# Performance work log

Hardware: AMD Instinct MI355X
Metric: run time of the kernel (lower is better)

The kernel has to match this reference:

```python
import jax, jax.numpy as jnp
import numpy as np
from jax import lax

B, T, D = 4, 4096, 1024  # d_inner == D (expansion=1.0)


def setup_inputs() -> dict:
    key = jax.random.key(0)
    ks = jax.random.split(key, 6)
    s = 1.0 / np.sqrt(D)  # xavier-ish scale
    return {
        "x": jax.random.normal(ks[0], (B, T, D), dtype=jnp.float32),
        "W_in": jax.random.normal(ks[1], (D, D), dtype=jnp.float32) * s,
        "W_alpha": jax.random.normal(ks[2], (D, D), dtype=jnp.float32) * s,
        "b_alpha": jnp.full((D,), 2.0, dtype=jnp.float32),
        "W_beta": jax.random.normal(ks[3], (D, D), dtype=jnp.float32) * s,
        "b_beta": jnp.zeros((D,), dtype=jnp.float32),
        "W_v": jax.random.normal(ks[4], (D, D), dtype=jnp.float32) * s,
        "b_v": jnp.zeros((D,), dtype=jnp.float32),
        "W_out": jax.random.normal(ks[5], (D, D), dtype=jnp.float32) * s,
    }


def reference(x, W_in, W_alpha, b_alpha, W_beta, b_beta, W_v, b_v, W_out):
    # x: [B, T, D]; torch nn.Linear convention y = x @ W.T
    xp = jax.nn.silu(jnp.einsum("btd,ed->bte", x, W_in))  # [B, T, Di]
    alpha = jax.nn.sigmoid(jnp.einsum("bte,fe->btf", xp, W_alpha) + b_alpha)
    beta = jax.nn.sigmoid(jnp.einsum("bte,fe->btf", xp, W_beta) + b_beta)
    v = jnp.tanh(jnp.einsum("bte,fe->btf", xp, W_v) + b_v)
    bv = beta * v  # precompute write term

    def step(h, ab):
        a_t, bv_t = ab  # each [B, Di]
        h = a_t * h + bv_t
        return h, h * jax.nn.silu(h)

    h0 = jnp.zeros((x.shape[0], W_alpha.shape[0]), dtype=x.dtype)
    h_last, outs = lax.scan(step, h0, (alpha.transpose(1, 0, 2), bv.transpose(1, 0, 2)))
    cell_out = outs.transpose(1, 0, 2)  # [B, T, Di]
    output = jnp.einsum("btf,df->btd", cell_out, W_out)
    return output, h_last
```

## Files before the change

### kernel.cpp

```cpp
#include <hip/hip_runtime.h>
#include <hip/hip_bf16.h>
#include <cstdint>
#include <cstddef>

typedef __bf16 bf16_t;
typedef _Float16 f16_t;
typedef __bf16 bf16x8 __attribute__((ext_vector_type(8)));
typedef float  f32x4  __attribute__((ext_vector_type(4)));
typedef float  f32x16 __attribute__((ext_vector_type(16)));

constexpr int kBatch = 4;
constexpr int kT = 4096;
constexpr int kD = 1024;
constexpr int kM = kBatch * kT;
constexpr int kCH = kBatch * kD;
constexpr int kNC = 128;
constexpr int kL  = kT / kNC;
constexpr int LDS_BYTES = 131072;

__device__ __forceinline__ void async16(const bf16_t* g, char* l) {
    __builtin_amdgcn_global_load_lds(
        (const __attribute__((address_space(1))) uint32_t*)g,
        (__attribute__((address_space(3))) uint32_t*)l,
        16, 0, 0);
}

__device__ __forceinline__ float fast_sigmoid(float z) {
    return 1.f / (1.f + __expf(-z));
}
__device__ __forceinline__ float fast_tanh(float z) {
    z = fminf(10.f, fmaxf(-10.f, z));
    float e = __expf(2.f * z);
    return (e - 1.f) / (e + 1.f);
}

__global__ void cvt_bf16_kernel(const float* __restrict__ in, bf16_t* __restrict__ out, int n8) {
    int i = blockIdx.x * blockDim.x + threadIdx.x;
    if (i >= n8) return;
    const float4* p = reinterpret_cast<const float4*>(in) + 2 * (size_t)i;
    float4 a = p[0], b = p[1];
    bf16x8 o;
    o[0] = (bf16_t)a.x; o[1] = (bf16_t)a.y; o[2] = (bf16_t)a.z; o[3] = (bf16_t)a.w;
    o[4] = (bf16_t)b.x; o[5] = (bf16_t)b.y; o[6] = (bf16_t)b.z; o[7] = (bf16_t)b.w;
    *reinterpret_cast<bf16x8*>(out + 8 * (size_t)i) = o;
}

__global__ void cvtw_kernel(const float* __restrict__ w0, const float* __restrict__ w1,
                            const float* __restrict__ w2, const float* __restrict__ w3,
                            const float* __restrict__ w4, bf16_t* __restrict__ out) {
    const int per = kD * kD / 8;
    int i = blockIdx.x * blockDim.x + threadIdx.x;
    int seg = i / per, j = i - seg * per;
    const float* src = seg == 0 ? w0 : seg == 1 ? w1 : seg == 2 ? w2 : seg == 3 ? w3 : w4;
    const float4* p = reinterpret_cast<const float4*>(src) + 2 * (size_t)j;
    float4 a = p[0], b = p[1];
    bf16x8 o;
    o[0] = (bf16_t)a.x; o[1] = (bf16_t)a.y; o[2] = (bf16_t)a.z; o[3] = (bf16_t)a.w;
    o[4] = (bf16_t)b.x; o[5] = (bf16_t)b.y; o[6] = (bf16_t)b.z; o[7] = (bf16_t)b.w;
    *reinterpret_cast<bf16x8*>(out + ((size_t)seg * per + j) * 8) = o;
}

template<int EPI>
__global__ __launch_bounds__(512, 2)
void gemm256(const bf16_t* __restrict__ A, const bf16_t* __restrict__ Bw,
             const float* __restrict__ bi0, const float* __restrict__ bi1,
             const float* __restrict__ bi2,
             void* __restrict__ out0, void* __restrict__ out1, void* __restrict__ out2,
             int M, int N, int K)
{
    extern __shared__ char lds[];
    const int tid  = threadIdx.x;
    const int lane = tid & 63;
    const int wv   = tid >> 6;
    const int wr   = wv >> 2;
    const int wc   = wv & 3;
    const int l32  = lane & 31;
    const int lh   = lane >> 5;

    int bid = blockIdx.y * gridDim.x + blockIdx.x;
    int nwg = gridDim.x * gridDim.y;
    int swz = (bid & 7) * (nwg >> 3) + (bid >> 3);
    int gx  = N >> 8;
    int n0  = (swz % gx) << 8;
    int m0  = (swz / gx) << 8;

    auto goff = [&](int chunk) -> size_t {
        int mb = (chunk >> 8) & 3;
        int ks = (chunk >> 6) & 3;
        int hl = (chunk >> 5) & 1;
        int r  = chunk & 31;
        return (size_t)(mb * 32 + r) * K + ks * 16 + hl * 8;
    };
    const size_t g0 = goff(tid), g1 = goff(512 + tid);
    const int d0 = wv << 10, d1 = 8192 + (wv << 10);

    auto STAGE = [&](const bf16_t* G, int row0, int k0, int lds_base) {
        const bf16_t* base = G + (size_t)row0 * K + k0;
        async16(base + g0, lds + lds_base + d0);
        async16(base + g1, lds + lds_base + d1);
    };
    auto STAGE_TILE = [&](int w, int bufo) {
        const int k0 = w << 6;
        STAGE(A,  m0,        k0, bufo);
        STAGE(A,  m0 + 128,  k0, bufo + 16384);
        STAGE(Bw, n0,        k0, bufo + 32768);
        STAGE(Bw, n0 + 128,  k0, bufo + 49152);
    };

    const int lane16 = lane << 4;
    int offA[4][4], offB[2][4];
#pragma unroll
    for (int m = 0; m < 4; ++m)
#pragma unroll
        for (int ks = 0; ks < 4; ++ks)
            offA[m][ks] = (m << 12) + (ks << 10) + lane16;
#pragma unroll
    for (int n = 0; n < 2; ++n)
#pragma unroll
        for (int ks = 0; ks < 4; ++ks)
            offB[n][ks] = ((((wc & 1) << 1) + n) << 12) + (ks << 10) + lane16;

    f32x16 acc[4][2];
#pragma unroll
    for (int i = 0; i < 4; ++i)
#pragma unroll
        for (int j = 0; j < 2; ++j)
            acc[i][j] = (f32x16)(0.f);

    const int NT = K >> 6;

    STAGE_TILE(0, 0);
    asm volatile("s_waitcnt vmcnt(0)" ::: "memory");
    asm volatile("s_barrier" ::: "memory");

    for (int w = 0; w < NT; ++w) {
        const int bufo  = (w & 1) << 16;
        const int nbufo = bufo ^ 65536;
        const int aReg = bufo + (wr << 14);
        const int bReg = bufo + 32768 + ((wc >> 1) << 14);

        if (w + 1 < NT) STAGE_TILE(w + 1, nbufo);

#pragma unroll
        for (int ks = 0; ks < 4; ++ks) {
            bf16x8 aF[4], bF[2];
#pragma unroll
            for (int m = 0; m < 4; ++m)
                aF[m] = *reinterpret_cast<const bf16x8*>(lds + aReg + offA[m][ks]);
#pragma unroll
            for (int n = 0; n < 2; ++n)
                bF[n] = *reinterpret_cast<const bf16x8*>(lds + bReg + offB[n][ks]);
            __builtin_amdgcn_s_setprio(1);
#pragma unroll
            for (int m = 0; m < 4; ++m)
#pragma unroll
                for (int n = 0; n < 2; ++n)
                    acc[m][n] = __builtin_amdgcn_mfma_f32_32x32x16_bf16(aF[m], bF[n], acc[m][n], 0, 0, 0);
            __builtin_amdgcn_s_setprio(0);
        }

        if (w + 1 < NT) {
            asm volatile("s_waitcnt vmcnt(0)" ::: "memory");
            asm volatile("s_barrier" ::: "memory");
        }
    }

    const int slab = n0 >> 10;
    const float* bia = (EPI == 4) ? (slab == 0 ? bi0 : slab == 1 ? bi1 : bi2) : nullptr;
#pragma unroll
    for (int nf = 0; nf < 2; ++nf) {
        const int colg = n0 + wc * 64 + nf * 32 + l32;
        const int cL = colg & (kD - 1);
        float bs = 0.f;
        if constexpr (EPI == 4) bs = bia[cL];
#pragma unroll
        for (int mf = 0; mf < 4; ++mf) {
            const int rbase = m0 + wr * 128 + mf * 32 + lh * 4;
#pragma unroll
            for (int rg = 0; rg < 16; ++rg) {
                const int rowg = rbase + (rg & 3) + ((rg >> 2) << 3);
                const float f = acc[mf][nf][rg];
                if constexpr (EPI == 0) {
                    float s = f * fast_sigmoid(f);
                    reinterpret_cast<bf16_t*>(out0)[(size_t)rowg * N + colg] = (bf16_t)s;
                } else if constexpr (EPI == 3) {
                    __builtin_nontemporal_store(f, reinterpret_cast<float*>(out0) + (size_t)rowg * N + colg);
                } else {
                    const size_t idx = (size_t)rowg * kD + cL;
                    if (slab == 0) {
                        reinterpret_cast<f16_t*>(out0)[idx] = (f16_t)fast_sigmoid(f + bs);
                    } else if (slab == 1) {
                        reinterpret_cast<bf16_t*>(out1)[idx] = (bf16_t)fast_sigmoid(f + bs);
                    } else {
                        reinterpret_cast<bf16_t*>(out2)[idx] = (bf16_t)fast_tanh(f + bs);
                    }
                }
            }
        }
    }
}

__global__ void scan_chunk_kernel(const f16_t* __restrict__ alpha,
                                  const bf16_t* __restrict__ beta,
                                  const bf16_t* __restrict__ vv,
                                  float* __restrict__ Aagg,
                                  float* __restrict__ Bagg)
{
    const int u  = blockIdx.x * blockDim.x + threadIdx.x;
    const int ch = u & (kCH - 1);
    const int c  = u >> 12;
    const int b  = ch >> 10;
    const int d  = ch & (kD - 1);
    size_t base = ((size_t)b * kT + (size_t)c * kL) * kD + d;
    float Ac = 1.f, Bc = 0.f;
#pragma unroll 4
    for (int t = 0; t < kL; ++t) {
        float a  = (float)alpha[base];
        float bv = (float)beta[base] * (float)vv[base];
        Ac *= a;
        Bc = a * Bc + bv;
        base += kD;
    }
    Aagg[u] = Ac;
    Bagg[u] = Bc;
}

__global__ void scan_mid_kernel(const float* __restrict__ Aagg,
                                const float* __restrict__ Bagg,
                                float* __restrict__ Hin,
                                float* __restrict__ hlast)
{
    const int ch = blockIdx.x * blockDim.x + threadIdx.x;
    float h = 0.f;
#pragma unroll 8
    for (int c = 0; c < kNC; ++c) {
        Hin[(size_t)c * kCH + ch] = h;
        h = Aagg[(size_t)c * kCH + ch] * h + Bagg[(size_t)c * kCH + ch];
    }
    hlast[ch] = h;
}

__global__ void scan_out_kernel(const f16_t* __restrict__ alpha,
                                const bf16_t* __restrict__ beta,
                                const bf16_t* __restrict__ vv,
                                const float* __restrict__ Hin,
                                bf16_t* __restrict__ cell)
{
    const int u  = blockIdx.x * blockDim.x + threadIdx.x;
    const int ch = u & (kCH - 1);
    const int c  = u >> 12;
    const int b  = ch >> 10;
    const int d  = ch & (kD - 1);
    size_t base = ((size_t)b * kT + (size_t)c * kL) * kD + d;
    float h = Hin[u];
#pragma unroll 4
    for (int t = 0; t < kL; ++t) {
        float a  = (float)alpha[base];
        float bv = (float)beta[base] * (float)vv[base];
        h = a * h + bv;
        float s = 1.f / (1.f + __expf(-h));
        cell[base] = (bf16_t)(h * h * s);
        base += kD;
    }
}

extern "C" void kernel_launch(void* const* d_in, const int* in_sizes, int n_in,
                              void* d_out, int out_size, void* d_ws, size_t ws_size,
                              hipStream_t stream)
{
    const float* x     = (const float*)d_in[0];
    const float* W_in  = (const float*)d_in[1];
    const float* W_al  = (const float*)d_in[2];
    const float* b_al  = (const float*)d_in[3];
    const float* W_be  = (const float*)d_in[4];
    const float* b_be  = (const float*)d_in[5];
    const float* W_v   = (const float*)d_in[6];
    const float* b_v   = (const float*)d_in[7];
    const float* W_out = (const float*)d_in[8];

    float* out   = (float*)d_out;
    float* hlast = out + (size_t)kM * kD;

    char* ws = (char*)d_ws;
    size_t off = 0;
    auto alloc = [&](size_t bytes) -> void* {
        void* p = ws + off;
        off += (bytes + 255) & ~(size_t)255;
        return p;
    };
    bf16_t* xbf   = (bf16_t*)alloc((size_t)kM * kD * 2);
    bf16_t* xp    = (bf16_t*)alloc((size_t)kM * kD * 2);
    f16_t*  alpha = (f16_t*) alloc((size_t)kM * kD * 2);
    bf16_t* betab = (bf16_t*)alloc((size_t)kM * kD * 2);
    bf16_t* vb    = (bf16_t*)alloc((size_t)kM * kD * 2);
    bf16_t* wbf   = (bf16_t*)alloc((size_t)5 * kD * kD * 2);

    bf16_t* Winb = wbf;
    bf16_t* Wfus = wbf + 1 * (size_t)kD * kD;
    bf16_t* Wob  = wbf + 4 * (size_t)kD * kD;

    bf16_t* cell = xbf;
    float*  Aagg = (float*)xp;
    float*  Bagg = Aagg + (size_t)kNC * kCH;
    float*  Hin  = Bagg + (size_t)kNC * kCH;

    hipFuncSetAttribute(reinterpret_cast<const void*>(gemm256<0>), hipFuncAttributeMaxDynamicSharedMemorySize, LDS_BYTES);
    hipFuncSetAttribute(reinterpret_cast<const void*>(gemm256<3>), hipFuncAttributeMaxDynamicSharedMemorySize, LDS_BYTES);
    hipFuncSetAttribute(reinterpret_cast<const void*>(gemm256<4>), hipFuncAttributeMaxDynamicSharedMemorySize, LDS_BYTES);

    {
        int n8 = kM * kD / 8;
        cvt_bf16_kernel<<<(n8 + 255) / 256, 256, 0, stream>>>(x, xbf, n8);
        int wtot = 5 * kD * kD / 8;
        cvtw_kernel<<<(wtot + 255) / 256, 256, 0, stream>>>(W_in, W_al, W_be, W_v, W_out, wbf);
    }

    dim3 grid1(kD / 256, kM / 256);
    dim3 gridF(3 * kD / 256, kM / 256);

    gemm256<0><<<grid1, 512, LDS_BYTES, stream>>>(xbf, Winb, nullptr, nullptr, nullptr,
                                                  xp, nullptr, nullptr, kM, kD, kD);
    gemm256<4><<<gridF, 512, LDS_BYTES, stream>>>(xp, Wfus, b_al, b_be, b_v,
                                                  alpha, betab, vb, kM, 3 * kD, kD);
    scan_chunk_kernel<<<kNC * kCH / 256, 256, 0, stream>>>(alpha, betab, vb, Aagg, Bagg);
    scan_mid_kernel<<<kCH / 256, 256, 0, stream>>>(Aagg, Bagg, Hin, hlast);
    scan_out_kernel<<<kNC * kCH / 256, 256, 0, stream>>>(alpha, betab, vb, Hin, cell);

    gemm256<3><<<grid1, 512, LDS_BYTES, stream>>>(cell, Wob, nullptr, nullptr, nullptr,
                                                  out, nullptr, nullptr, kM, kD, kD);
}
```

Before: 336.7 us.

## Store GEMM operands in pre-tiled LDS-matching layout for contiguous async loads

After: 324.8 us. -3.5%, faster.

```diff
diff --git a/kernel.cpp b/kernel.cpp
--- a/kernel.cpp
+++ b/kernel.cpp
@@ -5,6 +5,7 @@
 
 typedef __bf16 bf16_t;
 typedef _Float16 f16_t;
+typedef __bf16 bf16x4 __attribute__((ext_vector_type(4)));
 typedef __bf16 bf16x8 __attribute__((ext_vector_type(8)));
 typedef float  f32x4  __attribute__((ext_vector_type(4)));
 typedef float  f32x16 __attribute__((ext_vector_type(16)));
@@ -18,6 +19,12 @@
 constexpr int kL  = kT / kNC;
 constexpr int LDS_BYTES = 131072;
 
+__device__ __forceinline__ size_t tiled_idx(int r, int c, int ktiles ) {
+    return (size_t)((r >> 7) * ktiles + (c >> 6)) * 8192
+         + (((r >> 5) & 3) << 11) + (((c >> 4) & 3) << 9)
+         + (((c >> 3) & 1) << 8) + ((r & 31) << 3) + (c & 7);
+}
+
 __device__ __forceinline__ void async16(const bf16_t* g, char* l) {
     __builtin_amdgcn_global_load_lds(
         (const __attribute__((address_space(1))) uint32_t*)g,
@@ -34,30 +41,29 @@
     return (e - 1.f) / (e + 1.f);
 }
 
-__global__ void cvt_bf16_kernel(const float* __restrict__ in, bf16_t* __restrict__ out, int n8) {
-    int i = blockIdx.x * blockDim.x + threadIdx.x;
-    if (i >= n8) return;
-    const float4* p = reinterpret_cast<const float4*>(in) + 2 * (size_t)i;
-    float4 a = p[0], b = p[1];
-    bf16x8 o;
-    o[0] = (bf16_t)a.x; o[1] = (bf16_t)a.y; o[2] = (bf16_t)a.z; o[3] = (bf16_t)a.w;
-    o[4] = (bf16_t)b.x; o[5] = (bf16_t)b.y; o[6] = (bf16_t)b.z; o[7] = (bf16_t)b.w;
-    *reinterpret_cast<bf16x8*>(out + 8 * (size_t)i) = o;
-}
-
-__global__ void cvtw_kernel(const float* __restrict__ w0, const float* __restrict__ w1,
-                            const float* __restrict__ w2, const float* __restrict__ w3,
-                            const float* __restrict__ w4, bf16_t* __restrict__ out) {
-    const int per = kD * kD / 8;
-    int i = blockIdx.x * blockDim.x + threadIdx.x;
-    int seg = i / per, j = i - seg * per;
-    const float* src = seg == 0 ? w0 : seg == 1 ? w1 : seg == 2 ? w2 : seg == 3 ? w3 : w4;
-    const float4* p = reinterpret_cast<const float4*>(src) + 2 * (size_t)j;
-    float4 a = p[0], b = p[1];
-    bf16x8 o;
-    o[0] = (bf16_t)a.x; o[1] = (bf16_t)a.y; o[2] = (bf16_t)a.z; o[3] = (bf16_t)a.w;
-    o[4] = (bf16_t)b.x; o[5] = (bf16_t)b.y; o[6] = (bf16_t)b.z; o[7] = (bf16_t)b.w;
-    *reinterpret_cast<bf16x8*>(out + ((size_t)seg * per + j) * 8) = o;
+__global__ __launch_bounds__(256)
+void cvt_tiled_kernel(const float* __restrict__ src, bf16_t* __restrict__ dst) {
+    __shared__ __align__(16) bf16_t sl[8192];
+    const int tile = blockIdx.x;
+    const int rt = tile >> 4, kt = tile & 15;
+    const int tid = threadIdx.x;
+    const int c4 = tid & 15;
+    const int rl0 = tid >> 4;
+    const int coff = (((c4 >> 2) & 3) << 9) + (((c4 >> 1) & 1) << 8) + ((c4 & 1) << 2);
+#pragma unroll
+    for (int p = 0; p < 8; ++p) {
+        const int r = p * 16 + rl0;
+        float4 a = reinterpret_cast<const float4*>(src)[(size_t)(rt * 128 + r) * 256 + kt * 16 + c4];
+        bf16x4 o;
+        o[0] = (bf16_t)a.x; o[1] = (bf16_t)a.y; o[2] = (bf16_t)a.z; o[3] = (bf16_t)a.w;
+        *reinterpret_cast<bf16x4*>(&sl[((r >> 5) << 11) + ((r & 31) << 3) + coff]) = o;
+    }
+    __syncthreads();
+    bf16x8* d8 = reinterpret_cast<bf16x8*>(dst) + (size_t)tile * 1024;
+    const bf16x8* s8 = reinterpret_cast<const bf16x8*>(sl);
+#pragma unroll
+    for (int j = 0; j < 4; ++j)
+        d8[tid + j * 256] = s8[tid + j * 256];
 }
 
 template<int EPI>
@@ -84,18 +90,12 @@
     int n0  = (swz % gx) << 8;
     int m0  = (swz / gx) << 8;
 
-    auto goff = [&](int chunk) -> size_t {
-        int mb = (chunk >> 8) & 3;
-        int ks = (chunk >> 6) & 3;
-        int hl = (chunk >> 5) & 1;
-        int r  = chunk & 31;
-        return (size_t)(mb * 32 + r) * K + ks * 16 + hl * 8;
-    };
-    const size_t g0 = goff(tid), g1 = goff(512 + tid);
+    const int ktiles = K >> 6;
+    const size_t g0 = (size_t)tid * 8, g1 = (size_t)(512 + tid) * 8;
     const int d0 = wv << 10, d1 = 8192 + (wv << 10);
 
     auto STAGE = [&](const bf16_t* G, int row0, int k0, int lds_base) {
-        const bf16_t* base = G + (size_t)row0 * K + k0;
+        const bf16_t* base = G + (size_t)((row0 >> 7) * ktiles + (k0 >> 6)) * 8192;
         async16(base + g0, lds + lds_base + d0);
         async16(base + g1, lds + lds_base + d1);
     };
@@ -182,7 +182,7 @@
                 const float f = acc[mf][nf][rg];
                 if constexpr (EPI == 0) {
                     float s = f * fast_sigmoid(f);
-                    reinterpret_cast<bf16_t*>(out0)[(size_t)rowg * N + colg] = (bf16_t)s;
+                    reinterpret_cast<bf16_t*>(out0)[tiled_idx(rowg, colg, N >> 6)] = (bf16_t)s;
                 } else if constexpr (EPI == 3) {
                     __builtin_nontemporal_store(f, reinterpret_cast<float*>(out0) + (size_t)rowg * N + colg);
                 } else {
@@ -252,6 +252,11 @@
     const int b  = ch >> 10;
     const int d  = ch & (kD - 1);
     size_t base = ((size_t)b * kT + (size_t)c * kL) * kD + d;
+    const int rt = b * 32 + (c >> 2);
+    const int mb = (b * 128 + c) & 3;
+    const size_t tb = (size_t)(rt * 16 + (d >> 6)) * 8192
+                    + ((size_t)mb << 11) + (((d >> 4) & 3) << 9)
+                    + (((d >> 3) & 1) << 8) + (d & 7);
     float h = Hin[u];
 #pragma unroll 4
     for (int t = 0; t < kL; ++t) {
@@ -259,7 +264,7 @@
         float bv = (float)beta[base] * (float)vv[base];
         h = a * h + bv;
         float s = 1.f / (1.f + __expf(-h));
-        cell[base] = (bf16_t)(h * h * s);
+        cell[tb + t * 8] = (bf16_t)(h * h * s);
         base += kD;
     }
 }
@@ -308,12 +313,12 @@
     hipFuncSetAttribute(reinterpret_cast<const void*>(gemm256<3>), hipFuncAttributeMaxDynamicSharedMemorySize, LDS_BYTES);
     hipFuncSetAttribute(reinterpret_cast<const void*>(gemm256<4>), hipFuncAttributeMaxDynamicSharedMemorySize, LDS_BYTES);
 
-    {
-        int n8 = kM * kD / 8;
-        cvt_bf16_kernel<<<(n8 + 255) / 256, 256, 0, stream>>>(x, xbf, n8);
-        int wtot = 5 * kD * kD / 8;
-        cvtw_kernel<<<(wtot + 255) / 256, 256, 0, stream>>>(W_in, W_al, W_be, W_v, W_out, wbf);
-    }
+    cvt_tiled_kernel<<<kM / 128 * 16, 256, 0, stream>>>(x, xbf);
+    cvt_tiled_kernel<<<kD / 128 * 16, 256, 0, stream>>>(W_in,  Winb);
+    cvt_tiled_kernel<<<kD / 128 * 16, 256, 0, stream>>>(W_al,  wbf + 1 * (size_t)kD * kD);
+    cvt_tiled_kernel<<<kD / 128 * 16, 256, 0, stream>>>(W_be,  wbf + 2 * (size_t)kD * kD);
+    cvt_tiled_kernel<<<kD / 128 * 16, 256, 0, stream>>>(W_v,   wbf + 3 * (size_t)kD * kD);
+    cvt_tiled_kernel<<<kD / 128 * 16, 256, 0, stream>>>(W_out, Wob);
 
     dim3 grid1(kD / 256, kM / 256);
     dim3 gridF(3 * kD / 256, kM / 256);
```
